# Performance work log

Measured on AMD Instinct MI355X. Metric: run time of the kernel, lower is better.

## Reference

```python
import jax, jax.numpy as jnp
import numpy as np

B, S, D = 2, 2048, 1024
H, DH = 16, 64
N_CTX = 2048
IGNORE = -100000.0


def setup_inputs() -> dict:
    key = jax.random.key(0)
    ks = jax.random.split(key, 6)
    scale = 0.02
    return {
        "x": jax.random.normal(ks[0], (B, S, D), dtype=jnp.float32),
        "W_Q": jax.random.normal(ks[1], (H, DH, D), dtype=jnp.float32) * scale,
        "W_K": jax.random.normal(ks[2], (H, DH, D), dtype=jnp.float32) * scale,
        "W_V": jax.random.normal(ks[3], (H, DH, D), dtype=jnp.float32) * scale,
        "W_O": jax.random.normal(ks[4], (H, D, DH), dtype=jnp.float32) * scale,
        "b_Q": jnp.zeros((H, DH), dtype=jnp.float32),
        "b_K": jnp.zeros((H, DH), dtype=jnp.float32),
        "b_V": jnp.zeros((H, DH), dtype=jnp.float32),
        "b_O": jnp.zeros((D,), dtype=jnp.float32),
    }


def reference(x, W_Q, W_K, W_V, W_O, b_Q, b_K, b_V, b_O):
    attn_scale = jnp.sqrt(jnp.asarray(DH, dtype=x.dtype))
    # q,k,v: [batch, pos, head, d_head]
    q = jnp.einsum('ihm,bpm->bpih', W_Q, x) + b_Q
    k = jnp.einsum('ihm,bpm->bpih', W_K, x) + b_K
    v = jnp.einsum('ihm,bpm->bpih', W_V, x) + b_V
    # scores: [batch, head, q_pos, k_pos]
    attn_scores = jnp.einsum('bpih,bqih->bipq', q, k) / attn_scale
    # causal mask (pos_start=0, no kv cache)
    qs, ks_ = attn_scores.shape[-2], attn_scores.shape[-1]
    mask = jnp.tril(jnp.ones((qs, ks_), dtype=bool))
    attn_scores = jnp.where(mask, attn_scores, jnp.asarray(IGNORE, dtype=attn_scores.dtype))
    attn_matrix = jax.nn.softmax(attn_scores, axis=-1)
    # z: [batch, q_pos, head, d_head]
    z = jnp.einsum('bpih,biqp->bqih', v, attn_matrix)
    out = jnp.einsum('idh,bqih->bqd', W_O, z) + b_O
    return out
```

## Files before the change

kernel.cpp:

```cpp
#include <hip/hip_runtime.h>

typedef __bf16 bf16;
typedef __bf16 bf16x4 __attribute__((ext_vector_type(4)));
typedef __bf16 bf16x8 __attribute__((ext_vector_type(8)));
typedef float f32x4 __attribute__((ext_vector_type(4)));
typedef unsigned u32x4 __attribute__((ext_vector_type(4)));

#define AS1C(p) ((const __attribute__((address_space(1))) void*)(p))
#define AS3(p)  ((__attribute__((address_space(3))) void*)(p))

__device__ __forceinline__ void gld16(const bf16* gsrc, bf16* ldst) {
  __builtin_amdgcn_global_load_lds(AS1C(gsrc), AS3(ldst), 16, 0, 0);
}


__global__ void castx_kernel(const float* __restrict__ x, bf16* __restrict__ xb) {
  const int n4 = (4096 * 1024) / 4;
  for (int i = blockIdx.x * blockDim.x + threadIdx.x; i < n4; i += gridDim.x * blockDim.x) {
    float4 v = ((const float4*)x)[i];
    bf16x4 o;
    o[0] = (bf16)v.x; o[1] = (bf16)v.y; o[2] = (bf16)v.z; o[3] = (bf16)v.w;
    ((bf16x4*)xb)[i] = o;
  }
}

__global__ void prep_kernel(const float* __restrict__ WQ, const float* __restrict__ WK,
                            const float* __restrict__ WV, const float* __restrict__ WO,
                            const float* __restrict__ bQ, const float* __restrict__ bK,
                            const float* __restrict__ bV,
                            bf16* __restrict__ Wqkv, bf16* __restrict__ Wo2,
                            float* __restrict__ biasq) {
  const int WN = 1024 * 1024;
  const int total = 4 * WN + 3072;
  for (int i = blockIdx.x * blockDim.x + threadIdx.x; i < total; i += gridDim.x * blockDim.x) {
    if (i < WN) {
      Wqkv[i] = (bf16)(WQ[i] * 0.125f);
    } else if (i < 2 * WN) {
      Wqkv[i] = (bf16)WK[i - WN];
    } else if (i < 3 * WN) {
      Wqkv[i] = (bf16)WV[i - 2 * WN];
    } else if (i < 4 * WN) {
      int j = i - 3 * WN;
      int hh = j >> 16, r = j & 65535, d = r >> 6, dh = r & 63;
      Wo2[d * 1024 + hh * 64 + dh] = (bf16)WO[j];
    } else {
      int n = i - 4 * WN;
      biasq[n] = (n < 1024) ? bQ[n] * 0.125f : (n < 2048) ? bK[n - 1024] : bV[n - 2048];
    }
  }
}

template <int MODE>
__global__ __launch_bounds__(256, 2)
void gemm_bt(const bf16* __restrict__ A, const bf16* __restrict__ Bw,
             const float* __restrict__ bias,
             bf16* __restrict__ Qo, bf16* __restrict__ Ko, bf16* __restrict__ Vt,
             float* __restrict__ Co, int M, int N, int K) {
  __shared__ bf16 As[2][8192];
  __shared__ bf16 Bs[2][8192];
  const int tid = threadIdx.x;
  const int lane = tid & 63, w = tid >> 6;
  const int wr = w >> 1, wc = w & 1;
  const int g = lane >> 4, lr = lane & 15;
  const int perx = gridDim.x >> 3;
  const int tile = (blockIdx.x & 7) * perx + (blockIdx.x >> 3);
  const int brow = (tile & 31) * 128, bcol = (tile >> 5) * 128;

  auto stage = [&](int k0, int bufi) {
#pragma unroll
    for (int it = 0; it < 4; ++it) {
      const int cb = (it * 4 + w) * 64;
      const int u = cb + lane;
      const int lc = u ^ ((u >> 3) & 7);
      const int row = lc >> 3, c8 = (lc & 7) * 8;
      gld16(A + (size_t)(brow + row) * K + k0 + c8, &As[bufi][cb * 8]);
      gld16(Bw + (size_t)(bcol + row) * K + k0 + c8, &Bs[bufi][cb * 8]);
    }
  };

  f32x4 acc[4][4] = {};
  stage(0, 0);
  const int nstep = K >> 6;

  for (int t = 0; t < nstep; ++t) {
    __syncthreads();
    if (t + 1 < nstep) stage((t + 1) << 6, (t + 1) & 1);
    const bf16* as = As[t & 1];
    const bf16* bs = Bs[t & 1];
#pragma unroll
    for (int kk = 0; kk < 2; ++kk) {
      bf16x8 af[4], bfm[4];
#pragma unroll
      for (int m = 0; m < 4; ++m) {
        const int row = wr * 64 + m * 16 + lr;
        const int sl = (row * 8 + kk * 4 + g) ^ (lr & 7);
        af[m] = *(const bf16x8*)(as + sl * 8);
      }
#pragma unroll
      for (int n = 0; n < 4; ++n) {
        const int row = wc * 64 + n * 16 + lr;
        const int sl = (row * 8 + kk * 4 + g) ^ (lr & 7);
        bfm[n] = *(const bf16x8*)(bs + sl * 8);
      }
#pragma unroll
      for (int m = 0; m < 4; ++m)
#pragma unroll
        for (int n = 0; n < 4; ++n)
          acc[m][n] = __builtin_amdgcn_mfma_f32_16x16x32_bf16(af[m], bfm[n], acc[m][n], 0, 0, 0);
    }
  }

  const int row0 = brow + wr * 64;
  const int col0 = bcol + wc * 64;
#pragma unroll
  for (int m = 0; m < 4; ++m) {
#pragma unroll
    for (int n = 0; n < 4; ++n) {
      const int nidx = col0 + n * 16 + lr;
      f32x4 v = acc[m][n];
      const float bs = bias[nidx];
      if (MODE == 0) {
        const int stream = nidx >> 10;
        const int j = nidx & 1023;
        const int hh = j >> 6, dh = j & 63;
        const int r0 = row0 + m * 16 + g * 4;
        const int b = r0 >> 11;
        const int p0 = r0 & 2047;
        if (stream == 2) {
          bf16x4 vv;
#pragma unroll
          for (int i = 0; i < 4; ++i) vv[i] = (bf16)(v[i] + bs);
          *(bf16x4*)(Vt + ((size_t)(b * 16 + hh) * 64 + dh) * 2048 + p0) = vv;
        } else {
          bf16* dst = (stream == 0) ? Qo : Ko;
#pragma unroll
          for (int i = 0; i < 4; ++i)
            dst[((size_t)(b * 16 + hh) * 2048 + (p0 + i)) * 64 + dh] = (bf16)(v[i] + bs);
        }
      } else {
#pragma unroll
        for (int i = 0; i < 4; ++i) {
          const int r = row0 + m * 16 + g * 4 + i;
          Co[(size_t)r * 1024 + nidx] = v[i] + bs;
        }
      }
    }
  }
}

__global__ __launch_bounds__(256, 4)
void attn_kernel(const bf16* __restrict__ Qm, const bf16* __restrict__ Km,
                 const bf16* __restrict__ Vm, bf16* __restrict__ Z,
                 bf16* __restrict__ OP, float2* __restrict__ ML) {
  const int nblk = blockIdx.x;
  const int xcd = nblk & 7, s2 = nblk >> 3;
  const int Gl = s2 & 3, u = s2 >> 2;
  const int G = Gl * 8 + xcd;
  const int hh = G & 15, b = G >> 4;
  const int lane = threadIdx.x & 63, w = threadIdx.x >> 6;
  const int g = lane >> 4, lr = lane & 15;
  const bool g0 = g & 1, g1 = (g >> 1) & 1;

  int qt, t0, t1, spl;
  if (u < 32) {
    qt = 31 - (u >> 1); spl = u & 1;
    const int T = qt + 1, mid = (T + 1) >> 1;
    t0 = spl ? mid : 0; t1 = spl ? T : mid;
  } else {
    qt = 47 - u; spl = -1; t0 = 0; t1 = qt + 1;
  }

  __shared__ bf16 Ks[2][4096];
  __shared__ bf16 Vs[2][4096];

  const bf16* Qb = Qm + (size_t)G * 2048 * 64;
  const bf16* Kb = Km + (size_t)G * 2048 * 64;
  const bf16* Vb = Vm + (size_t)G * 64 * 2048;

  auto stage = [&](int kv0, int bufi) {
#pragma unroll
    for (int it = 0; it < 2; ++it) {
      const int cb = w * 128 + it * 64;
      const int uu = cb + lane;
      const int lc = uu ^ ((uu >> 3) & 7);
      const int row = lc >> 3, c8 = (lc & 7) * 8;
      gld16(Kb + (size_t)(kv0 + row) * 64 + c8, &Ks[bufi][cb * 8]);
      gld16(Vb + (size_t)row * 2048 + kv0 + c8, &Vs[bufi][cb * 8]);
    }
  };

  const int q0w = qt * 64 + w * 16;
  const int qg = q0w + lr;

  bf16x8 aq[2];
#pragma unroll
  for (int kk = 0; kk < 2; ++kk)
    aq[kk] = *(const bf16x8*)(Qb + (size_t)qg * 64 + kk * 32 + g * 8);

  float m_i = -1e30f, l_i = 0.f;
  f32x4 oacc[4] = {};

  int buf = 0;
  stage(t0 * 64, 0);
  __syncthreads();

  for (int t = t0; t < t1; ++t) {
    if (t + 1 < t1) stage((t + 1) * 64, buf ^ 1);
    const int kv0 = t * 64;

    f32x4 s[4] = {};
#pragma unroll
    for (int kk = 0; kk < 2; ++kk) {
#pragma unroll
      for (int n = 0; n < 4; ++n) {
        const int r = n * 16 + lr;
        const int sl = (r * 8 + kk * 4 + g) ^ (r & 7);
        bf16x8 bk = *(const bf16x8*)(&Ks[buf][sl * 8]);
        s[n] = __builtin_amdgcn_mfma_f32_16x16x32_bf16(bk, aq[kk], s[n], 0, 0, 0);
      }
    }
    if (t == qt) {
#pragma unroll
      for (int n = 0; n < 4; ++n)
#pragma unroll
        for (int i = 0; i < 4; ++i)
          if (kv0 + n * 16 + g * 4 + i > qg) s[n][i] = -1e9f;
    }

    float tm = fmaxf(fmaxf(fmaxf(s[0][0], s[0][1]), fmaxf(s[0][2], s[0][3])),
                     fmaxf(fmaxf(s[1][0], s[1][1]), fmaxf(s[1][2], s[1][3])));
    tm = fmaxf(tm, fmaxf(fmaxf(fmaxf(s[2][0], s[2][1]), fmaxf(s[2][2], s[2][3])),
                         fmaxf(fmaxf(s[3][0], s[3][1]), fmaxf(s[3][2], s[3][3]))));
    tm = fmaxf(tm, __shfl_xor(tm, 16));
    tm = fmaxf(tm, __shfl_xor(tm, 32));
    const float mn = fmaxf(m_i, tm);
    const float al = __expf(m_i - mn);
    m_i = mn;
#pragma unroll
    for (int n = 0; n < 4; ++n)
#pragma unroll
      for (int i = 0; i < 4; ++i) s[n][i] = __expf(s[n][i] - mn);
    float ts = ((s[0][0] + s[0][1]) + (s[0][2] + s[0][3])) +
               ((s[1][0] + s[1][1]) + (s[1][2] + s[1][3])) +
               ((s[2][0] + s[2][1]) + (s[2][2] + s[2][3])) +
               ((s[3][0] + s[3][1]) + (s[3][2] + s[3][3]));
    ts += __shfl_xor(ts, 16);
    ts += __shfl_xor(ts, 32);
    l_i = l_i * al + ts;
#pragma unroll
    for (int n = 0; n < 4; ++n)
#pragma unroll
      for (int i = 0; i < 4; ++i) oacc[n][i] *= al;

    unsigned U[8];
#pragma unroll
    for (int n = 0; n < 4; ++n)
#pragma unroll
      for (int h = 0; h < 2; ++h) {
        unsigned lo = (unsigned)__builtin_bit_cast(unsigned short, (bf16)s[n][2 * h]);
        unsigned hi = (unsigned)__builtin_bit_cast(unsigned short, (bf16)s[n][2 * h + 1]);
        U[n * 2 + h] = lo | (hi << 16);
      }
    unsigned rA0 = (unsigned)__shfl_xor((int)(g1 ? U[0] : U[2]), 32);
    unsigned rA1 = (unsigned)__shfl_xor((int)(g1 ? U[1] : U[3]), 32);
    unsigned rA2 = (unsigned)__shfl_xor((int)(g1 ? U[4] : U[6]), 32);
    unsigned rA3 = (unsigned)__shfl_xor((int)(g1 ? U[5] : U[7]), 32);
    unsigned v2_000 = g1 ? rA0 : U[0];
    unsigned v2_001 = g1 ? rA1 : U[1];
    unsigned v2_010 = g1 ? U[2] : rA0;
    unsigned v2_011 = g1 ? U[3] : rA1;
    unsigned v2_100 = g1 ? rA2 : U[4];
    unsigned v2_101 = g1 ? rA3 : U[5];
    unsigned v2_110 = g1 ? U[6] : rA2;
    unsigned v2_111 = g1 ? U[7] : rA3;
    unsigned rB0 = (unsigned)__shfl_xor((int)(g0 ? v2_000 : v2_010), 16);
    unsigned rB1 = (unsigned)__shfl_xor((int)(g0 ? v2_001 : v2_011), 16);
    unsigned rB2 = (unsigned)__shfl_xor((int)(g0 ? v2_100 : v2_110), 16);
    unsigned rB3 = (unsigned)__shfl_xor((int)(g0 ? v2_101 : v2_111), 16);
    u32x4 t0v, t1v;
    t0v[0] = g0 ? rB0 : v2_000;
    t0v[1] = g0 ? rB1 : v2_001;
    t0v[2] = g0 ? v2_010 : rB0;
    t0v[3] = g0 ? v2_011 : rB1;
    t1v[0] = g0 ? rB2 : v2_100;
    t1v[1] = g0 ? rB3 : v2_101;
    t1v[2] = g0 ? v2_110 : rB2;
    t1v[3] = g0 ? v2_111 : rB3;
    bf16x8 pb0 = __builtin_bit_cast(bf16x8, t0v);
    bf16x8 pb1 = __builtin_bit_cast(bf16x8, t1v);

#pragma unroll
    for (int kk = 0; kk < 2; ++kk) {
      const bf16x8 pb = kk ? pb1 : pb0;
#pragma unroll
      for (int n = 0; n < 4; ++n) {
        const int r = n * 16 + lr;
        const int sl = (r * 8 + kk * 4 + g) ^ (r & 7);
        bf16x8 av = *(const bf16x8*)(&Vs[buf][sl * 8]);
        oacc[n] = __builtin_amdgcn_mfma_f32_16x16x32_bf16(av, pb, oacc[n], 0, 0, 0);
      }
    }
    __syncthreads();
    buf ^= 1;
  }

  if (u < 32) {
    const int pr = G * 1024 + (qt - 16) * 64 + w * 16 + lr;
    bf16* oprow = OP + (size_t)(spl * 32768 + pr) * 64;
#pragma unroll
    for (int n = 0; n < 4; ++n) {
      bf16x4 o4;
#pragma unroll
      for (int i = 0; i < 4; ++i) o4[i] = (bf16)oacc[n][i];
      *(bf16x4*)(oprow + n * 16 + g * 4) = o4;
    }
    if (lane < 16) ML[spl * 32768 + pr] = make_float2(m_i, l_i);
  } else {
    const float li = 1.f / l_i;
    bf16* zrow = Z + ((size_t)(b * 2048 + qg) * 16 + hh) * 64;
#pragma unroll
    for (int n = 0; n < 4; ++n) {
      bf16x4 o4;
#pragma unroll
      for (int i = 0; i < 4; ++i) o4[i] = (bf16)(oacc[n][i] * li);
      *(bf16x4*)(zrow + n * 16 + g * 4) = o4;
    }
  }
}

__global__ __launch_bounds__(256)
void combine_kernel(const bf16* __restrict__ OP, const float2* __restrict__ ML,
                    bf16* __restrict__ Z) {
  const int id = blockIdx.x * 256 + threadIdx.x;
  const int pr = id >> 3, d8 = id & 7;
  const float2 ml0 = ML[pr], ml1 = ML[32768 + pr];
  const float m = fmaxf(ml0.x, ml1.x);
  const float w0 = __expf(ml0.x - m), w1 = __expf(ml1.x - m);
  const float inv = 1.f / (ml0.y * w0 + ml1.y * w1);
  const bf16x8 a = *(const bf16x8*)(OP + (size_t)pr * 64 + d8 * 8);
  const bf16x8 c = *(const bf16x8*)(OP + ((size_t)32768 + pr) * 64 + d8 * 8);
  bf16x8 o;
#pragma unroll
  for (int j = 0; j < 8; ++j)
    o[j] = (bf16)(((float)a[j] * w0 + (float)c[j] * w1) * inv);
  const int bh = pr >> 10, qr = pr & 1023;
  const int bb = bh >> 4, hq = bh & 15;
  *(bf16x8*)(Z + (((size_t)(bb * 2048 + 1024 + qr)) * 16 + hq) * 64 + d8 * 8) = o;
}

extern "C" void kernel_launch(void* const* d_in, const int* in_sizes, int n_in,
                              void* d_out, int out_size, void* d_ws, size_t ws_size,
                              hipStream_t stream) {
  const float* x  = (const float*)d_in[0];
  const float* WQ = (const float*)d_in[1];
  const float* WK = (const float*)d_in[2];
  const float* WV = (const float*)d_in[3];
  const float* WO = (const float*)d_in[4];
  const float* bQ = (const float*)d_in[5];
  const float* bK = (const float*)d_in[6];
  const float* bV = (const float*)d_in[7];
  const float* bO = (const float*)d_in[8];
  float* out = (float*)d_out;

  char* ws = (char*)d_ws;
  bf16* xb    = (bf16*)(ws);
  bf16* Wqkv  = (bf16*)(ws + (8u << 20));
  bf16* Wo2   = (bf16*)(ws + (14u << 20));
  bf16* Qb    = (bf16*)(ws + (16u << 20));
  bf16* Kb    = (bf16*)(ws + (24u << 20));
  bf16* Vtb   = (bf16*)(ws + (32u << 20));
  bf16* Zb    = (bf16*)(ws + (40u << 20));
  float* biasq = (float*)(ws + (48u << 20));
  bf16* OP    = (bf16*)(ws);
  float2* ML  = (float2*)(ws + (8u << 20));

  castx_kernel<<<2048, 256, 0, stream>>>(x, xb);
  prep_kernel<<<2048, 256, 0, stream>>>(WQ, WK, WV, WO, bQ, bK, bV, Wqkv, Wo2, biasq);
  gemm_bt<0><<<768, 256, 0, stream>>>(xb, Wqkv, biasq, Qb, Kb, Vtb, nullptr,
                                      4096, 3072, 1024);
  attn_kernel<<<1536, 256, 0, stream>>>(Qb, Kb, Vtb, Zb, OP, ML);
  combine_kernel<<<1024, 256, 0, stream>>>(OP, ML, Zb);
  gemm_bt<1><<<256, 256, 0, stream>>>(Zb, Wo2, bO, nullptr, nullptr, nullptr, out,
                                      4096, 1024, 1024);
}
```

Baseline: 207.4 us.

## Merge prep kernels, persist QKV GEMM over two tiles, deepen load pipeline

Fuses the x-cast and weight-prep kernels into one launch. The QKV GEMM now runs 512 blocks instead of 768, and the first 256 blocks each process a second tile, so the grid fits a single wave. The K-loop switches to explicit vmcnt waits and raw barriers, with a prefetch distance of two k-steps, and it stages the next tile's first loads before the epilogue. The aim is to cut launch overhead and the tail effect of a partial second wave, and to hide global-load latency. The cost is an uneven per-block load (some blocks do twice the work) and fragile hand-written waitcnt accounting.

```diff
diff --git a/kernel.cpp b/kernel.cpp
--- a/kernel.cpp
+++ b/kernel.cpp
@@ -14,38 +14,38 @@
 }
 
 
-__global__ void castx_kernel(const float* __restrict__ x, bf16* __restrict__ xb) {
-  const int n4 = (4096 * 1024) / 4;
-  for (int i = blockIdx.x * blockDim.x + threadIdx.x; i < n4; i += gridDim.x * blockDim.x) {
-    float4 v = ((const float4*)x)[i];
-    bf16x4 o;
-    o[0] = (bf16)v.x; o[1] = (bf16)v.y; o[2] = (bf16)v.z; o[3] = (bf16)v.w;
-    ((bf16x4*)xb)[i] = o;
-  }
-}
-
-__global__ void prep_kernel(const float* __restrict__ WQ, const float* __restrict__ WK,
-                            const float* __restrict__ WV, const float* __restrict__ WO,
-                            const float* __restrict__ bQ, const float* __restrict__ bK,
-                            const float* __restrict__ bV,
-                            bf16* __restrict__ Wqkv, bf16* __restrict__ Wo2,
-                            float* __restrict__ biasq) {
+__global__ void prep_all(const float* __restrict__ x,
+                         const float* __restrict__ WQ, const float* __restrict__ WK,
+                         const float* __restrict__ WV, const float* __restrict__ WO,
+                         const float* __restrict__ bQ, const float* __restrict__ bK,
+                         const float* __restrict__ bV,
+                         bf16* __restrict__ xb, bf16* __restrict__ Wqkv,
+                         bf16* __restrict__ Wo2, float* __restrict__ biasq) {
+  const int X4 = (4096 * 1024) / 4;
   const int WN = 1024 * 1024;
-  const int total = 4 * WN + 3072;
+  const int total = X4 + 4 * WN + 3072;
   for (int i = blockIdx.x * blockDim.x + threadIdx.x; i < total; i += gridDim.x * blockDim.x) {
-    if (i < WN) {
-      Wqkv[i] = (bf16)(WQ[i] * 0.125f);
-    } else if (i < 2 * WN) {
-      Wqkv[i] = (bf16)WK[i - WN];
-    } else if (i < 3 * WN) {
-      Wqkv[i] = (bf16)WV[i - 2 * WN];
-    } else if (i < 4 * WN) {
-      int j = i - 3 * WN;
-      int hh = j >> 16, r = j & 65535, d = r >> 6, dh = r & 63;
-      Wo2[d * 1024 + hh * 64 + dh] = (bf16)WO[j];
+    if (i < X4) {
+      float4 v = ((const float4*)x)[i];
+      bf16x4 o;
+      o[0] = (bf16)v.x; o[1] = (bf16)v.y; o[2] = (bf16)v.z; o[3] = (bf16)v.w;
+      ((bf16x4*)xb)[i] = o;
     } else {
-      int n = i - 4 * WN;
-      biasq[n] = (n < 1024) ? bQ[n] * 0.125f : (n < 2048) ? bK[n - 1024] : bV[n - 2048];
+      int j = i - X4;
+      if (j < WN) {
+        Wqkv[j] = (bf16)(WQ[j] * 0.125f);
+      } else if (j < 2 * WN) {
+        Wqkv[j] = (bf16)WK[j - WN];
+      } else if (j < 3 * WN) {
+        Wqkv[j] = (bf16)WV[j - 2 * WN];
+      } else if (j < 4 * WN) {
+        int k = j - 3 * WN;
+        int hh = k >> 16, r = k & 65535, d = r >> 6, dh = r & 63;
+        Wo2[d * 1024 + hh * 64 + dh] = (bf16)WO[k];
+      } else {
+        int n = j - 4 * WN;
+        biasq[n] = (n < 1024) ? bQ[n] * 0.125f : (n < 2048) ? bK[n - 1024] : bV[n - 2048];
+      }
     }
   }
 }
@@ -62,86 +62,105 @@
   const int lane = tid & 63, w = tid >> 6;
   const int wr = w >> 1, wc = w & 1;
   const int g = lane >> 4, lr = lane & 15;
-  const int perx = gridDim.x >> 3;
-  const int tile = (blockIdx.x & 7) * perx + (blockIdx.x >> 3);
-  const int brow = (tile & 31) * 128, bcol = (tile >> 5) * 128;
-
-  auto stage = [&](int k0, int bufi) {
+  const int nstep = K >> 6;
+
+  const int xcd = blockIdx.x & 7, loc = blockIdx.x >> 3;
+  int tiles[2];
+  int nt = 1;
+  tiles[0] = xcd * (gridDim.x >> 3) + loc;
+  if (MODE == 0 && blockIdx.x < 256) { tiles[1] = 512 + xcd * 32 + loc; nt = 2; }
+
+  auto stageT = [&](int tile, int t, int bufi) {
+    const int br = (tile & 31) * 128, bc = (tile >> 5) * 128;
+    const int k0 = t << 6;
 #pragma unroll
     for (int it = 0; it < 4; ++it) {
       const int cb = (it * 4 + w) * 64;
       const int u = cb + lane;
       const int lc = u ^ ((u >> 3) & 7);
       const int row = lc >> 3, c8 = (lc & 7) * 8;
-      gld16(A + (size_t)(brow + row) * K + k0 + c8, &As[bufi][cb * 8]);
-      gld16(Bw + (size_t)(bcol + row) * K + k0 + c8, &Bs[bufi][cb * 8]);
+      gld16(A + (size_t)(br + row) * K + k0 + c8, &As[bufi][cb * 8]);
+      gld16(Bw + (size_t)(bc + row) * K + k0 + c8, &Bs[bufi][cb * 8]);
     }
   };
 
-  f32x4 acc[4][4] = {};
-  stage(0, 0);
-  const int nstep = K >> 6;
-
-  for (int t = 0; t < nstep; ++t) {
-    __syncthreads();
-    if (t + 1 < nstep) stage((t + 1) << 6, (t + 1) & 1);
-    const bf16* as = As[t & 1];
-    const bf16* bs = Bs[t & 1];
-#pragma unroll
-    for (int kk = 0; kk < 2; ++kk) {
-      bf16x8 af[4], bfm[4];
-#pragma unroll
-      for (int m = 0; m < 4; ++m) {
-        const int row = wr * 64 + m * 16 + lr;
-        const int sl = (row * 8 + kk * 4 + g) ^ (lr & 7);
-        af[m] = *(const bf16x8*)(as + sl * 8);
-      }
+  stageT(tiles[0], 0, 0);
+  stageT(tiles[0], 1, 1);
+
+  for (int ti = 0; ti < nt; ++ti) {
+    const int tile = tiles[ti];
+    const int brow = (tile & 31) * 128, bcol = (tile >> 5) * 128;
+    f32x4 acc[4][4] = {};
+
+    for (int t = 0; t < nstep; ++t) {
+      if (t + 1 < nstep) { asm volatile("s_waitcnt vmcnt(8)" ::: "memory"); }
+      else               { asm volatile("s_waitcnt vmcnt(0)" ::: "memory"); }
+      __builtin_amdgcn_sched_barrier(0);
+      __builtin_amdgcn_s_barrier();
+
+      const bf16* as = As[t & 1];
+      const bf16* bs = Bs[t & 1];
+#pragma unroll
+      for (int kk = 0; kk < 2; ++kk) {
+        bf16x8 af[4], bfm[4];
+#pragma unroll
+        for (int m = 0; m < 4; ++m) {
+          const int row = wr * 64 + m * 16 + lr;
+          const int sl = (row * 8 + kk * 4 + g) ^ (lr & 7);
+          af[m] = *(const bf16x8*)(as + sl * 8);
+        }
+#pragma unroll
+        for (int n = 0; n < 4; ++n) {
+          const int row = wc * 64 + n * 16 + lr;
+          const int sl = (row * 8 + kk * 4 + g) ^ (lr & 7);
+          bfm[n] = *(const bf16x8*)(bs + sl * 8);
+        }
+#pragma unroll
+        for (int m = 0; m < 4; ++m)
+#pragma unroll
+          for (int n = 0; n < 4; ++n)
+            acc[m][n] = __builtin_amdgcn_mfma_f32_16x16x32_bf16(af[m], bfm[n], acc[m][n], 0, 0, 0);
+      }
+      __builtin_amdgcn_sched_barrier(0);
+      __builtin_amdgcn_s_barrier();
+      if (t + 2 < nstep) stageT(tile, t + 2, t & 1);
+    }
+
+    if (ti + 1 < nt) { stageT(tiles[ti + 1], 0, 0); stageT(tiles[ti + 1], 1, 1); }
+
+    const int row0 = brow + wr * 64;
+    const int col0 = bcol + wc * 64;
+#pragma unroll
+    for (int m = 0; m < 4; ++m) {
 #pragma unroll
       for (int n = 0; n < 4; ++n) {
-        const int row = wc * 64 + n * 16 + lr;
-        const int sl = (row * 8 + kk * 4 + g) ^ (lr & 7);
-        bfm[n] = *(const bf16x8*)(bs + sl * 8);
-      }
-#pragma unroll
-      for (int m = 0; m < 4; ++m)
-#pragma unroll
-        for (int n = 0; n < 4; ++n)
-          acc[m][n] = __builtin_amdgcn_mfma_f32_16x16x32_bf16(af[m], bfm[n], acc[m][n], 0, 0, 0);
-    }
-  }
-
-  const int row0 = brow + wr * 64;
-  const int col0 = bcol + wc * 64;
-#pragma unroll
-  for (int m = 0; m < 4; ++m) {
-#pragma unroll
-    for (int n = 0; n < 4; ++n) {
-      const int nidx = col0 + n * 16 + lr;
-      f32x4 v = acc[m][n];
-      const float bs = bias[nidx];
-      if (MODE == 0) {
-        const int stream = nidx >> 10;
-        const int j = nidx & 1023;
-        const int hh = j >> 6, dh = j & 63;
-        const int r0 = row0 + m * 16 + g * 4;
-        const int b = r0 >> 11;
-        const int p0 = r0 & 2047;
-        if (stream == 2) {
-          bf16x4 vv;
-#pragma unroll
-          for (int i = 0; i < 4; ++i) vv[i] = (bf16)(v[i] + bs);
-          *(bf16x4*)(Vt + ((size_t)(b * 16 + hh) * 64 + dh) * 2048 + p0) = vv;
+        const int nidx = col0 + n * 16 + lr;
+        f32x4 v = acc[m][n];
+        const float bs = bias[nidx];
+        if (MODE == 0) {
+          const int stream = nidx >> 10;
+          const int j = nidx & 1023;
+          const int hh = j >> 6, dh = j & 63;
+          const int r0 = row0 + m * 16 + g * 4;
+          const int b = r0 >> 11;
+          const int p0 = r0 & 2047;
+          if (stream == 2) {
+            bf16x4 vv;
+#pragma unroll
+            for (int i = 0; i < 4; ++i) vv[i] = (bf16)(v[i] + bs);
+            *(bf16x4*)(Vt + ((size_t)(b * 16 + hh) * 64 + dh) * 2048 + p0) = vv;
+          } else {
+            bf16* dst = (stream == 0) ? Qo : Ko;
+#pragma unroll
+            for (int i = 0; i < 4; ++i)
+              dst[((size_t)(b * 16 + hh) * 2048 + (p0 + i)) * 64 + dh] = (bf16)(v[i] + bs);
+          }
         } else {
-          bf16* dst = (stream == 0) ? Qo : Ko;
-#pragma unroll
-          for (int i = 0; i < 4; ++i)
-            dst[((size_t)(b * 16 + hh) * 2048 + (p0 + i)) * 64 + dh] = (bf16)(v[i] + bs);
-        }
-      } else {
-#pragma unroll
-        for (int i = 0; i < 4; ++i) {
-          const int r = row0 + m * 16 + g * 4 + i;
-          Co[(size_t)r * 1024 + nidx] = v[i] + bs;
+#pragma unroll
+          for (int i = 0; i < 4; ++i) {
+            const int r = row0 + m * 16 + g * 4 + i;
+            Co[(size_t)r * 1024 + nidx] = v[i] + bs;
+          }
         }
       }
     }
@@ -374,9 +393,8 @@
   bf16* OP    = (bf16*)(ws);
   float2* ML  = (float2*)(ws + (8u << 20));
 
-  castx_kernel<<<2048, 256, 0, stream>>>(x, xb);
-  prep_kernel<<<2048, 256, 0, stream>>>(WQ, WK, WV, WO, bQ, bK, bV, Wqkv, Wo2, biasq);
-  gemm_bt<0><<<768, 256, 0, stream>>>(xb, Wqkv, biasq, Qb, Kb, Vtb, nullptr,
+  prep_all<<<2048, 256, 0, stream>>>(x, WQ, WK, WV, WO, bQ, bK, bV, xb, Wqkv, Wo2, biasq);
+  gemm_bt<0><<<512, 256, 0, stream>>>(xb, Wqkv, biasq, Qb, Kb, Vtb, nullptr,
                                       4096, 3072, 1024);
   attn_kernel<<<1536, 256, 0, stream>>>(Qb, Kb, Vtb, Zb, OP, ML);
   combine_kernel<<<1024, 256, 0, stream>>>(OP, ML, Zb);
```

Measured after the change: 203.9 us. About the same (-1.7%).
